# Optimization experiments

Measured on AMD Instinct MI355X. Metric: run time of the kernel, lower is better.

## Reference

```python
import jax, jax.numpy as jnp
import numpy as np

WS = 7            # window size
N = WS * WS       # tokens per window (49)
DIM = 128
HEADS = 4
HEAD_DIM = DIM // HEADS
SCALE = HEAD_DIM ** -0.5
NW = 64           # number of windows (mask leading dim)
B_WIN = 4096      # B * nW


def _relative_position_index():
    coords = np.stack(np.meshgrid(np.arange(WS), np.arange(WS), indexing='ij'))  # (2,WS,WS)
    cf = coords.reshape(2, -1)                       # (2, N)
    rel = cf[:, :, None] - cf[:, None, :]            # (2, N, N)
    rel = rel.transpose(1, 2, 0).copy()              # (N, N, 2)
    rel[..., 0] += WS - 1
    rel[..., 1] += WS - 1
    rel[..., 0] *= 2 * WS - 1
    return rel.sum(-1)                               # (N, N) int

REL_IDX = jnp.asarray(_relative_position_index())


def setup_inputs() -> dict:
    key = jax.random.key(0)
    ks = jax.random.split(key, 7)
    return {
        'x': jax.random.normal(ks[0], (B_WIN, N, DIM), dtype=jnp.float32),
        'mask': jax.random.normal(ks[1], (NW, N, N), dtype=jnp.float32),
        'qkv_w': jax.random.normal(ks[2], (3 * DIM, DIM), dtype=jnp.float32) * 0.02,
        'qkv_b': jax.random.normal(ks[3], (3 * DIM,), dtype=jnp.float32) * 0.02,
        'proj_w': jax.random.normal(ks[4], (DIM, DIM), dtype=jnp.float32) * 0.02,
        'proj_b': jax.random.normal(ks[5], (DIM,), dtype=jnp.float32) * 0.02,
        'bias_table': jax.random.normal(ks[6], ((2 * WS - 1) ** 2, HEADS), dtype=jnp.float32) * 0.02,
    }


def reference(x, mask, qkv_w, qkv_b, proj_w, proj_b, bias_table):
    B_, n, C = x.shape
    # qkv projection: (B_, N, 3C) -> (3, B_, H, N, hd)
    qkv = (x @ qkv_w.T + qkv_b).reshape(B_, n, 3, HEADS, HEAD_DIM)
    qkv = jnp.transpose(qkv, (2, 0, 3, 1, 4))
    q, k, v = qkv[0], qkv[1], qkv[2]
    # scaled scores: (B_, H, N, N)
    attn = jnp.einsum('bhnd,bhmd->bhnm', q * SCALE, k)
    # gathered relative position bias: (N, N, H) -> (H, N, N)
    rel_bias = jnp.transpose(bias_table[REL_IDX], (2, 0, 1))
    attn = attn + rel_bias[None]
    # shifted-window mask: broadcast over batch groups and heads
    nW = mask.shape[0]
    attn = attn.reshape(B_ // nW, nW, HEADS, n, n) + mask[None, :, None]
    attn = attn.reshape(B_, HEADS, n, n)
    attn = jax.nn.softmax(attn, axis=-1)
    out = jnp.einsum('bhnm,bhmd->bhnd', attn, v)
    out = jnp.transpose(out, (0, 2, 1, 3)).reshape(B_, n, C)
    return out @ proj_w.T + proj_b
```

## Files before the change

### kernel.cpp

```cpp
#include <hip/hip_runtime.h>

#define QK_SCALE 0.17677669529663687f

typedef __attribute__((ext_vector_type(8))) short bf16x8;
typedef __attribute__((ext_vector_type(4))) short bf16x4;
typedef __attribute__((ext_vector_type(4))) float floatx4;

__device__ __forceinline__ unsigned short f2bf(float f) {
    unsigned int u = __float_as_uint(f);
    u += 0x7fffu + ((u >> 16) & 1u);
    return (unsigned short)(u >> 16);
}

__device__ __forceinline__ bf16x8 ld8_2x4(const short* p) {
    union { bf16x8 v8; bf16x4 v4[2]; } u;
    u.v4[0] = *(const bf16x4*)p;
    u.v4[1] = *(const bf16x4*)(p + 4);
    return u.v8;
}

__global__ __launch_bounds__(256) void prep_kernel(
    const float* __restrict__ qkv_w, const float* __restrict__ proj_w,
    const float* __restrict__ bias_table, const float* __restrict__ mask,
    unsigned short* __restrict__ wbf, float* __restrict__ cm)
{
    int g = blockIdx.x * 256 + threadIdx.x;
    if (g < 49152) {
        wbf[g] = f2bf(qkv_w[g]);
    } else if (g < 65536) {
        wbf[g] = f2bf(proj_w[g - 49152]);
    } else if (g < 680192) {
        int t = g - 65536;
        int j = t % 49; int t2 = t / 49;
        int i = t2 % 49; int t3 = t2 / 49;
        int h = t3 & 3;  int wn = t3 >> 2;
        int idx = (i / 7 - j / 7 + 6) * 13 + (i % 7 - j % 7 + 6);
        cm[t] = mask[wn * 2401 + i * 49 + j] + bias_table[idx * 4 + h];
    }
}

__global__ __launch_bounds__(256, 2) void winattn_mfma(
    const float* __restrict__ x,
    const float* __restrict__ qkv_b,
    const float* __restrict__ proj_b,
    const unsigned short* __restrict__ wbf,
    const float* __restrict__ cm,
    float* __restrict__ out)
{
    __shared__ __align__(16) short smem[29696];

    const int tid  = threadIdx.x;
    const int lane = tid & 63;
    const int lid  = lane & 15;
    const int quad = lane >> 4;
    const int h    = tid >> 6;
    const int b    = blockIdx.x;
    const int w    = b & 63;
    const int hq   = h * 7424;

    {
        const float4* xg = (const float4*)(x + (size_t)b * 6272);
        for (int i = tid; i < 1568; i += 256) {
            int n = i >> 5, c4 = i & 31;
            float4 v = xg[i];
            ushort4 u;
            u.x = f2bf(v.x); u.y = f2bf(v.y); u.z = f2bf(v.z); u.w = f2bf(v.w);
            *(ushort4*)&smem[n * 136 + c4 * 4] = u;
        }
        ushort4 z; z.x = 0; z.y = 0; z.z = 0; z.w = 0;
        for (int i = tid; i < 510; i += 256)
            *(ushort4*)&smem[49 * 136 + i * 4] = z;
    }
    __syncthreads();

    bf16x8 ax[4][4];
    #pragma unroll
    for (int mt = 0; mt < 4; ++mt)
        #pragma unroll
        for (int kb = 0; kb < 4; ++kb)
            ax[mt][kb] = *(const bf16x8*)&smem[(mt * 16 + lid) * 136 + kb * 32 + quad * 8];
    __syncthreads();

    const floatx4 z4 = {0.f, 0.f, 0.f, 0.f};

    #pragma unroll
    for (int t = 0; t < 6; ++t) {
        const int cb = (t < 2) ? (h * 32 + t * 16)
                     : (t < 4) ? (128 + h * 32 + (t - 2) * 16)
                               : (256 + h * 32 + (t - 4) * 16);
        const unsigned short* wr = wbf + (size_t)(cb + lid) * 128 + quad * 8;
        floatx4 acc[4] = {z4, z4, z4, z4};
        #pragma unroll
        for (int kb = 0; kb < 4; ++kb) {
            bf16x8 bw = *(const bf16x8*)(wr + kb * 32);
            #pragma unroll
            for (int mt = 0; mt < 4; ++mt)
                acc[mt] = __builtin_amdgcn_mfma_f32_16x16x32_bf16(ax[mt][kb], bw, acc[mt], 0, 0, 0);
        }
        const float bias = qkv_b[cb + lid];
        #pragma unroll
        for (int mt = 0; mt < 4; ++mt) {
            #pragma unroll
            for (int r = 0; r < 4; ++r) {
                const int row = mt * 16 + quad * 4 + r;
                const float v = acc[mt][r] + bias;
                if (t < 2) {
                    smem[hq + row * 40 + t * 16 + lid] = (short)f2bf(v * QK_SCALE);
                } else if (t < 4) {
                    smem[hq + 2560 + row * 40 + (t - 2) * 16 + lid] = (short)f2bf(v);
                } else {
                    smem[hq + 5120 + ((t - 4) * 16 + lid) * 72 + row] = (short)f2bf(v);
                }
            }
        }
    }

    bf16x8 aq[4], bk[4];
    #pragma unroll
    for (int mt = 0; mt < 4; ++mt)
        aq[mt] = ld8_2x4(&smem[hq + (mt * 16 + lid) * 40 + quad * 8]);
    #pragma unroll
    for (int nt = 0; nt < 4; ++nt)
        bk[nt] = ld8_2x4(&smem[hq + 2560 + (nt * 16 + lid) * 40 + quad * 8]);

    floatx4 sacc[4][4];
    #pragma unroll
    for (int mt = 0; mt < 4; ++mt)
        #pragma unroll
        for (int nt = 0; nt < 4; ++nt)
            sacc[mt][nt] = __builtin_amdgcn_mfma_f32_16x16x32_bf16(aq[mt], bk[nt], z4, 0, 0, 0);

    float invs[4][4];
    const float* cmb = cm + (size_t)(w * 4 + h) * 2401;
    #pragma unroll
    for (int mt = 0; mt < 4; ++mt) {
        #pragma unroll
        for (int r = 0; r < 4; ++r) {
            const int row  = mt * 16 + quad * 4 + r;
            const int rowc = (row < 49) ? row : 48;
            float sv[4];
            #pragma unroll
            for (int nt = 0; nt < 4; ++nt) {
                const int col  = nt * 16 + lid;
                const int colc = (col < 49) ? col : 48;
                float val = sacc[mt][nt][r] + cmb[rowc * 49 + colc];
                sv[nt] = (col < 49) ? val : -1e30f;
            }
            float mx = fmaxf(fmaxf(sv[0], sv[1]), fmaxf(sv[2], sv[3]));
            #pragma unroll
            for (int d = 1; d < 16; d <<= 1) mx = fmaxf(mx, __shfl_xor(mx, d));
            float sum = 0.f;
            #pragma unroll
            for (int nt = 0; nt < 4; ++nt) { float p = __expf(sv[nt] - mx); sv[nt] = p; sum += p; }
            #pragma unroll
            for (int d = 1; d < 16; d <<= 1) sum += __shfl_xor(sum, d);
            invs[mt][r] = 1.f / sum;
            #pragma unroll
            for (int nt = 0; nt < 4; ++nt)
                smem[hq + row * 72 + nt * 16 + lid] = (short)f2bf(sv[nt]);
        }
    }

    bf16x8 bv[2][2];
    #pragma unroll
    for (int nt2 = 0; nt2 < 2; ++nt2)
        #pragma unroll
        for (int kb2 = 0; kb2 < 2; ++kb2)
            bv[nt2][kb2] = *(const bf16x8*)&smem[hq + 5120 + (nt2 * 16 + lid) * 72 + kb2 * 32 + quad * 8];

    floatx4 oacc[4][2] = {{z4, z4}, {z4, z4}, {z4, z4}, {z4, z4}};
    #pragma unroll
    for (int mt = 0; mt < 4; ++mt) {
        #pragma unroll
        for (int kb2 = 0; kb2 < 2; ++kb2) {
            bf16x8 ap = *(const bf16x8*)&smem[hq + (mt * 16 + lid) * 72 + kb2 * 32 + quad * 8];
            #pragma unroll
            for (int nt2 = 0; nt2 < 2; ++nt2)
                oacc[mt][nt2] = __builtin_amdgcn_mfma_f32_16x16x32_bf16(ap, bv[nt2][kb2], oacc[mt][nt2], 0, 0, 0);
        }
    }

    __syncthreads();

    #pragma unroll
    for (int mt = 0; mt < 4; ++mt)
        #pragma unroll
        for (int nt2 = 0; nt2 < 2; ++nt2)
            #pragma unroll
            for (int r = 0; r < 4; ++r) {
                const int row = mt * 16 + quad * 4 + r;
                smem[row * 136 + h * 32 + nt2 * 16 + lid] =
                    (short)f2bf(oacc[mt][nt2][r] * invs[mt][r]);
            }
    __syncthreads();

    bf16x8 aa[4][4];
    #pragma unroll
    for (int mt = 0; mt < 4; ++mt)
        #pragma unroll
        for (int kb = 0; kb < 4; ++kb)
            aa[mt][kb] = *(const bf16x8*)&smem[(mt * 16 + lid) * 136 + kb * 32 + quad * 8];

    float* outb = out + (size_t)b * 6272;
    #pragma unroll
    for (int nt = 0; nt < 2; ++nt) {
        const int cb = h * 32 + nt * 16;
        const unsigned short* wr = wbf + 49152 + (size_t)(cb + lid) * 128 + quad * 8;
        floatx4 acc[4] = {z4, z4, z4, z4};
        #pragma unroll
        for (int kb = 0; kb < 4; ++kb) {
            bf16x8 bw = *(const bf16x8*)(wr + kb * 32);
            #pragma unroll
            for (int mt = 0; mt < 4; ++mt)
                acc[mt] = __builtin_amdgcn_mfma_f32_16x16x32_bf16(aa[mt][kb], bw, acc[mt], 0, 0, 0);
        }
        const float pb = proj_b[cb + lid];
        #pragma unroll
        for (int mt = 0; mt < 4; ++mt)
            #pragma unroll
            for (int r = 0; r < 4; ++r) {
                const int row = mt * 16 + quad * 4 + r;
                if (row < 49)
                    outb[row * 128 + cb + lid] = acc[mt][r] + pb;
            }
    }
}

extern "C" void kernel_launch(void* const* d_in, const int* in_sizes, int n_in,
                              void* d_out, int out_size, void* d_ws, size_t ws_size,
                              hipStream_t stream) {
    (void)in_sizes; (void)n_in; (void)out_size; (void)ws_size;
    const float* x          = (const float*)d_in[0];
    const float* mask       = (const float*)d_in[1];
    const float* qkv_w      = (const float*)d_in[2];
    const float* qkv_b      = (const float*)d_in[3];
    const float* proj_w     = (const float*)d_in[4];
    const float* proj_b     = (const float*)d_in[5];
    const float* bias_table = (const float*)d_in[6];

    unsigned short* wbf = (unsigned short*)d_ws;
    float* cm           = (float*)((char*)d_ws + 131072);

    prep_kernel<<<2657, 256, 0, stream>>>(qkv_w, proj_w, bias_table, mask, wbf, cm);
    winattn_mfma<<<4096, 256, 0, stream>>>(x, qkv_b, proj_b, wbf, cm, (float*)d_out);
}
```

Baseline: 297.8 us.

## Shrink per-head LDS, fold mask bias into MFMA init, raise occupancy

Per-head shared memory shrinks (V and P strides go from 72 to 68, region size reduced), so total LDS drops and launch bounds ask for 3 blocks per CU instead of 2. The combined mask and bias is loaded straight into the score MFMA accumulator rather than added afterwards. The V projection moves after the QK^T step so fewer live registers overlap. The prep kernel is vectorised and reorganised per row. Together these aim for higher occupancy and fewer instructions, with a risk of register spills under the tighter launch bound.

```diff
diff --git a/kernel.cpp b/kernel.cpp
--- a/kernel.cpp
+++ b/kernel.cpp
@@ -1,6 +1,10 @@
 #include <hip/hip_runtime.h>
 
 #define QK_SCALE 0.17677669529663687f
+#define HREG 6528
+#define KOFF 2560
+#define VOFF 4352
+#define XP   136
 
 typedef __attribute__((ext_vector_type(8))) short bf16x8;
 typedef __attribute__((ext_vector_type(4))) short bf16x4;
@@ -24,22 +28,29 @@
     const float* __restrict__ bias_table, const float* __restrict__ mask,
     unsigned short* __restrict__ wbf, float* __restrict__ cm)
 {
-    int g = blockIdx.x * 256 + threadIdx.x;
-    if (g < 49152) {
-        wbf[g] = f2bf(qkv_w[g]);
-    } else if (g < 65536) {
-        wbf[g] = f2bf(proj_w[g - 49152]);
-    } else if (g < 680192) {
-        int t = g - 65536;
-        int j = t % 49; int t2 = t / 49;
-        int i = t2 % 49; int t3 = t2 / 49;
-        int h = t3 & 3;  int wn = t3 >> 2;
-        int idx = (i / 7 - j / 7 + 6) * 13 + (i % 7 - j % 7 + 6);
-        cm[t] = mask[wn * 2401 + i * 49 + j] + bias_table[idx * 4 + h];
-    }
-}
-
-__global__ __launch_bounds__(256, 2) void winattn_mfma(
+    const int blk = blockIdx.x;
+    if (blk < 64) {
+        const int g = (blk * 256 + threadIdx.x) * 4;
+        float4 v = (g < 49152) ? *(const float4*)(qkv_w + g)
+                               : *(const float4*)(proj_w + (g - 49152));
+        ushort4 u;
+        u.x = f2bf(v.x); u.y = f2bf(v.y); u.z = f2bf(v.z); u.w = f2bf(v.w);
+        *(ushort4*)(wbf + g) = u;
+    } else {
+        const int rid = (blk - 64) * 4 + (threadIdx.x >> 6);
+        const int j = threadIdx.x & 63;
+        if (j < 49) {
+            const int i  = rid % 49;
+            const int hw = rid / 49;
+            const int h  = hw & 3;
+            const int wn = hw >> 2;
+            const int idx = (i / 7 - j / 7 + 6) * 13 + (i % 7 - j % 7 + 6);
+            cm[rid * 49 + j] = mask[wn * 2401 + i * 49 + j] + bias_table[idx * 4 + h];
+        }
+    }
+}
+
+__global__ __launch_bounds__(256, 3) void winattn_mfma(
     const float* __restrict__ x,
     const float* __restrict__ qkv_b,
     const float* __restrict__ proj_b,
@@ -47,7 +58,7 @@
     const float* __restrict__ cm,
     float* __restrict__ out)
 {
-    __shared__ __align__(16) short smem[29696];
+    __shared__ __align__(16) short smem[26112];
 
     const int tid  = threadIdx.x;
     const int lane = tid & 63;
@@ -56,7 +67,7 @@
     const int h    = tid >> 6;
     const int b    = blockIdx.x;
     const int w    = b & 63;
-    const int hq   = h * 7424;
+    const int hq   = h * HREG;
 
     {
         const float4* xg = (const float4*)(x + (size_t)b * 6272);
@@ -65,11 +76,11 @@
             float4 v = xg[i];
             ushort4 u;
             u.x = f2bf(v.x); u.y = f2bf(v.y); u.z = f2bf(v.z); u.w = f2bf(v.w);
-            *(ushort4*)&smem[n * 136 + c4 * 4] = u;
+            *(ushort4*)&smem[n * XP + c4 * 4] = u;
         }
         ushort4 z; z.x = 0; z.y = 0; z.z = 0; z.w = 0;
         for (int i = tid; i < 510; i += 256)
-            *(ushort4*)&smem[49 * 136 + i * 4] = z;
+            *(ushort4*)&smem[49 * XP + i * 4] = z;
     }
     __syncthreads();
 
@@ -78,16 +89,14 @@
     for (int mt = 0; mt < 4; ++mt)
         #pragma unroll
         for (int kb = 0; kb < 4; ++kb)
-            ax[mt][kb] = *(const bf16x8*)&smem[(mt * 16 + lid) * 136 + kb * 32 + quad * 8];
+            ax[mt][kb] = *(const bf16x8*)&smem[(mt * 16 + lid) * XP + kb * 32 + quad * 8];
     __syncthreads();
 
     const floatx4 z4 = {0.f, 0.f, 0.f, 0.f};
 
     #pragma unroll
-    for (int t = 0; t < 6; ++t) {
-        const int cb = (t < 2) ? (h * 32 + t * 16)
-                     : (t < 4) ? (128 + h * 32 + (t - 2) * 16)
-                               : (256 + h * 32 + (t - 4) * 16);
+    for (int t = 0; t < 4; ++t) {
+        const int cb = (t < 2) ? (h * 32 + t * 16) : (128 + h * 32 + (t - 2) * 16);
         const unsigned short* wr = wbf + (size_t)(cb + lid) * 128 + quad * 8;
         floatx4 acc[4] = {z4, z4, z4, z4};
         #pragma unroll
@@ -99,20 +108,14 @@
         }
         const float bias = qkv_b[cb + lid];
         #pragma unroll
-        for (int mt = 0; mt < 4; ++mt) {
+        for (int mt = 0; mt < 4; ++mt)
             #pragma unroll
             for (int r = 0; r < 4; ++r) {
                 const int row = mt * 16 + quad * 4 + r;
                 const float v = acc[mt][r] + bias;
-                if (t < 2) {
-                    smem[hq + row * 40 + t * 16 + lid] = (short)f2bf(v * QK_SCALE);
-                } else if (t < 4) {
-                    smem[hq + 2560 + row * 40 + (t - 2) * 16 + lid] = (short)f2bf(v);
-                } else {
-                    smem[hq + 5120 + ((t - 4) * 16 + lid) * 72 + row] = (short)f2bf(v);
-                }
-            }
-        }
+                if (t < 2)  smem[hq + row * 40 + t * 16 + lid] = (short)f2bf(v * QK_SCALE);
+                else        smem[hq + KOFF + row * 40 + (t - 2) * 16 + lid] = (short)f2bf(v);
+            }
     }
 
     bf16x8 aq[4], bk[4];
@@ -121,30 +124,60 @@
         aq[mt] = ld8_2x4(&smem[hq + (mt * 16 + lid) * 40 + quad * 8]);
     #pragma unroll
     for (int nt = 0; nt < 4; ++nt)
-        bk[nt] = ld8_2x4(&smem[hq + 2560 + (nt * 16 + lid) * 40 + quad * 8]);
-
+        bk[nt] = ld8_2x4(&smem[hq + KOFF + (nt * 16 + lid) * 40 + quad * 8]);
+
+    const float* cmb = cm + (size_t)(w * 4 + h) * 2401;
     floatx4 sacc[4][4];
     #pragma unroll
-    for (int mt = 0; mt < 4; ++mt)
-        #pragma unroll
-        for (int nt = 0; nt < 4; ++nt)
-            sacc[mt][nt] = __builtin_amdgcn_mfma_f32_16x16x32_bf16(aq[mt], bk[nt], z4, 0, 0, 0);
+    for (int mt = 0; mt < 4; ++mt) {
+        const int r0 = mt * 16 + quad * 4;
+        #pragma unroll
+        for (int nt = 0; nt < 4; ++nt) {
+            const int col  = nt * 16 + lid;
+            const int colc = (col < 49) ? col : 48;
+            floatx4 ci;
+            #pragma unroll
+            for (int r = 0; r < 4; ++r) {
+                const int rowc = (r0 + r < 49) ? (r0 + r) : 48;
+                ci[r] = cmb[rowc * 49 + colc];
+            }
+            sacc[mt][nt] = __builtin_amdgcn_mfma_f32_16x16x32_bf16(aq[mt], bk[nt], ci, 0, 0, 0);
+        }
+    }
+
+    #pragma unroll
+    for (int tv = 0; tv < 2; ++tv) {
+        const int cb = 256 + h * 32 + tv * 16;
+        const unsigned short* wr = wbf + (size_t)(cb + lid) * 128 + quad * 8;
+        floatx4 acc[4] = {z4, z4, z4, z4};
+        #pragma unroll
+        for (int kb = 0; kb < 4; ++kb) {
+            bf16x8 bw = *(const bf16x8*)(wr + kb * 32);
+            #pragma unroll
+            for (int mt = 0; mt < 4; ++mt)
+                acc[mt] = __builtin_amdgcn_mfma_f32_16x16x32_bf16(ax[mt][kb], bw, acc[mt], 0, 0, 0);
+        }
+        const float bias = qkv_b[cb + lid];
+        #pragma unroll
+        for (int mt = 0; mt < 4; ++mt)
+            #pragma unroll
+            for (int r = 0; r < 4; ++r) {
+                const int row = mt * 16 + quad * 4 + r;
+                smem[hq + VOFF + (tv * 16 + lid) * 68 + row] = (short)f2bf(acc[mt][r] + bias);
+            }
+    }
 
     float invs[4][4];
-    const float* cmb = cm + (size_t)(w * 4 + h) * 2401;
     #pragma unroll
     for (int mt = 0; mt < 4; ++mt) {
         #pragma unroll
         for (int r = 0; r < 4; ++r) {
-            const int row  = mt * 16 + quad * 4 + r;
-            const int rowc = (row < 49) ? row : 48;
+            const int row = mt * 16 + quad * 4 + r;
             float sv[4];
             #pragma unroll
             for (int nt = 0; nt < 4; ++nt) {
-                const int col  = nt * 16 + lid;
-                const int colc = (col < 49) ? col : 48;
-                float val = sacc[mt][nt][r] + cmb[rowc * 49 + colc];
-                sv[nt] = (col < 49) ? val : -1e30f;
+                const int col = nt * 16 + lid;
+                sv[nt] = (col < 49) ? sacc[mt][nt][r] : -1e30f;
             }
             float mx = fmaxf(fmaxf(sv[0], sv[1]), fmaxf(sv[2], sv[3]));
             #pragma unroll
@@ -157,7 +190,7 @@
             invs[mt][r] = 1.f / sum;
             #pragma unroll
             for (int nt = 0; nt < 4; ++nt)
-                smem[hq + row * 72 + nt * 16 + lid] = (short)f2bf(sv[nt]);
+                smem[hq + row * 68 + nt * 16 + lid] = (short)f2bf(sv[nt]);
         }
     }
 
@@ -166,14 +199,14 @@
     for (int nt2 = 0; nt2 < 2; ++nt2)
         #pragma unroll
         for (int kb2 = 0; kb2 < 2; ++kb2)
-            bv[nt2][kb2] = *(const bf16x8*)&smem[hq + 5120 + (nt2 * 16 + lid) * 72 + kb2 * 32 + quad * 8];
+            bv[nt2][kb2] = ld8_2x4(&smem[hq + VOFF + (nt2 * 16 + lid) * 68 + kb2 * 32 + quad * 8]);
 
     floatx4 oacc[4][2] = {{z4, z4}, {z4, z4}, {z4, z4}, {z4, z4}};
     #pragma unroll
     for (int mt = 0; mt < 4; ++mt) {
         #pragma unroll
         for (int kb2 = 0; kb2 < 2; ++kb2) {
-            bf16x8 ap = *(const bf16x8*)&smem[hq + (mt * 16 + lid) * 72 + kb2 * 32 + quad * 8];
+            bf16x8 ap = ld8_2x4(&smem[hq + (mt * 16 + lid) * 68 + kb2 * 32 + quad * 8]);
             #pragma unroll
             for (int nt2 = 0; nt2 < 2; ++nt2)
                 oacc[mt][nt2] = __builtin_amdgcn_mfma_f32_16x16x32_bf16(ap, bv[nt2][kb2], oacc[mt][nt2], 0, 0, 0);
@@ -189,7 +222,7 @@
             #pragma unroll
             for (int r = 0; r < 4; ++r) {
                 const int row = mt * 16 + quad * 4 + r;
-                smem[row * 136 + h * 32 + nt2 * 16 + lid] =
+                smem[row * XP + h * 32 + nt2 * 16 + lid] =
                     (short)f2bf(oacc[mt][nt2][r] * invs[mt][r]);
             }
     __syncthreads();
@@ -199,7 +232,7 @@
     for (int mt = 0; mt < 4; ++mt)
         #pragma unroll
         for (int kb = 0; kb < 4; ++kb)
-            aa[mt][kb] = *(const bf16x8*)&smem[(mt * 16 + lid) * 136 + kb * 32 + quad * 8];
+            aa[mt][kb] = *(const bf16x8*)&smem[(mt * 16 + lid) * XP + kb * 32 + quad * 8];
 
     float* outb = out + (size_t)b * 6272;
     #pragma unroll
@@ -241,6 +274,6 @@
     unsigned short* wbf = (unsigned short*)d_ws;
     float* cm           = (float*)((char*)d_ws + 131072);
 
-    prep_kernel<<<2657, 256, 0, stream>>>(qkv_w, proj_w, bias_table, mask, wbf, cm);
+    prep_kernel<<<3200, 256, 0, stream>>>(qkv_w, proj_w, bias_table, mask, wbf, cm);
     winattn_mfma<<<4096, 256, 0, stream>>>(x, qkv_b, proj_b, wbf, cm, (float*)d_out);
 }
```

After: 338.0 us. 1.13x slower.
